# Performance work log

Measured on AMD Instinct MI355X. Metric: run time of the kernel, lower is better.

## Reference

```python
import jax, jax.numpy as jnp
import numpy as np
import math

N_USR = 50000
N_ENT = 100000
D = 64
N_REL = 16
E = 1_000_000
EI = 500_000
N_HEADS = 2


def setup_inputs() -> dict:
    key = jax.random.key(0)
    ks = jax.random.split(key, 9)
    user_emb = jax.random.normal(ks[0], (N_USR, D), jnp.float32) * 0.1
    entity_emb = jax.random.normal(ks[1], (N_ENT, D), jnp.float32) * 0.1
    edge_index = jax.random.randint(ks[2], (2, E), 0, N_ENT, dtype=jnp.int32)
    edge_type = jax.random.randint(ks[3], (E,), 1, N_REL + 1, dtype=jnp.int32)  # values in [1, N_REL]
    inter_u = jax.random.randint(ks[4], (EI,), 0, N_USR, dtype=jnp.int32)
    inter_i = jax.random.randint(ks[5], (EI,), 0, N_ENT, dtype=jnp.int32)
    inter_edge = jnp.stack([inter_u, inter_i], axis=0)
    inter_edge_w = jax.random.uniform(ks[6], (EI,), jnp.float32)
    relation_emb = jax.random.normal(ks[7], (N_REL, D), jnp.float32) * 0.1
    W_Q = jax.random.normal(ks[8], (D, D), jnp.float32) * 0.1
    return {
        'layers_num': 2,
        'user_emb': user_emb,
        'entity_emb': entity_emb,
        'inter_edge': inter_edge,
        'inter_edge_w': inter_edge_w,
        'edge_index': edge_index,
        'edge_type': edge_type,
        'relation_emb': relation_emb,
        'W_Q': W_Q,
    }


def _scatter_softmax(scores, idx, n_segments):
    # scores: [E, H]; softmax over edges sharing the same head index
    m = jax.ops.segment_max(scores, idx, num_segments=n_segments)  # [n, H]
    ex = jnp.exp(scores - m[idx])
    denom = jax.ops.segment_sum(ex, idx, num_segments=n_segments)
    return ex / denom[idx]


def reference(layers_num, user_emb, entity_emb, inter_edge, inter_edge_w, edge_index, edge_type, relation_emb, W_Q):
    n_entities = entity_emb.shape[0]
    n_users = user_emb.shape[0]
    d = entity_emb.shape[1]
    h = N_HEADS
    dk = d // h
    head, tail = edge_index[0], edge_index[1]
    iu, ii = inter_edge[0], inter_edge[1]

    def agg_layer(u_emb, e_emb):
        rel = relation_emb[edge_type - 1]                                # [E, d]
        query = (e_emb[head] @ W_Q).reshape(-1, h, dk)                   # [E, h, dk]
        key = (e_emb[tail] @ W_Q).reshape(-1, h, dk) * rel.reshape(-1, h, dk)
        score = (query * key).sum(-1) / math.sqrt(dk)                    # [E, h]
        attn = _scatter_softmax(score, head, n_entities)                 # [E, h]
        value = (e_emb[tail] * rel).reshape(-1, h, dk)                   # [E, h, dk]
        entity_agg = (value * attn[:, :, None]).reshape(-1, d)           # [E, d]
        entity_agg = jax.ops.segment_sum(entity_agg, head, num_segments=n_entities)
        # F.normalize (L2, eps=1e-12)
        norm = jnp.sqrt(jnp.sum(entity_agg * entity_agg, axis=1, keepdims=True))
        entity_agg = entity_agg / jnp.maximum(norm, 1e-12)
        item_agg = inter_edge_w[:, None] * e_emb[ii]                      # [Ei, d]
        user_agg = jax.ops.segment_sum(item_agg, iu, num_segments=n_users)
        return entity_agg, user_agg

    user_embs = [user_emb]
    entity_embs = [entity_emb]
    u, e = user_emb, entity_emb
    for _ in range(layers_num):
        e, u = agg_layer(u, e)
        user_embs.append(u)
        entity_embs.append(e)
    user_out = jnp.mean(jnp.stack(user_embs, axis=1), axis=1)
    entity_out = jnp.mean(jnp.stack(entity_embs, axis=1), axis=1)
    return (user_out, entity_out)
```

## Files before the change

### kernel.cpp

```cpp
#include <hip/hip_runtime.h>
#include <hip/hip_fp16.h>
#include <math.h>

#define N_USR 50000
#define N_ENT 100000
#define DIM   64
#define NE    1000000
#define NEI   500000

#define BKW   125
#define EBK   800
#define UBK   400
#define CAP   1664
#define KCH   4096
#define NBA_E 245
#define NBA_U 123

#define NBE_B 12500
#define NBU_B 6250

__device__ __forceinline__ __half2 pick_lo(unsigned a, unsigned b) {
    unsigned r = __builtin_amdgcn_perm(b, a, 0x05040100u);
    return *(__half2*)&r;
}
__device__ __forceinline__ __half2 pick_hi(unsigned a, unsigned b) {
    unsigned r = __builtin_amdgcn_perm(b, a, 0x07060302u);
    return *(__half2*)&r;
}

template <int CTRL>
__device__ __forceinline__ float dpp_add(float x) {
    int y = __builtin_amdgcn_update_dpp(0, __builtin_bit_cast(int, x),
                                        CTRL, 0xF, 0xF, true);
    return x + __builtin_bit_cast(float, y);
}

__device__ __forceinline__ int swz16_maxi(int x) {
    int t = __builtin_amdgcn_ds_swizzle(x, 0x401F);
    return max(x, t);
}

typedef _Float16 fp16x2 __attribute__((ext_vector_type(2)));
typedef _Float16 half8 __attribute__((ext_vector_type(8)));
typedef float floatx4 __attribute__((ext_vector_type(4)));

__device__ __forceinline__ float dot2(__half2 a, __half2 b, float c) {
#if __has_builtin(__builtin_amdgcn_fdot2)
    return __builtin_amdgcn_fdot2(__builtin_bit_cast(fp16x2, a),
                                  __builtin_bit_cast(fp16x2, b), c, false);
#else
    __half2 m = __hmul2(a, b);
    return c + __low2float(m) + __high2float(m);
#endif
}

__device__ __forceinline__ float exp2_fast(float x) {
#if __has_builtin(__builtin_amdgcn_exp2f)
    return __builtin_amdgcn_exp2f(x);
#else
    return exp2f(x);
#endif
}

__global__ __launch_bounds__(256) void k_gemm(const float* __restrict__ Emat,
                                              const float* __restrict__ WQ,
                                              unsigned int* __restrict__ Gu,
                                              int ntiles) {
    int lane = threadIdx.x & 63;
    int tile = (int)((blockIdx.x * 256 + threadIdx.x) >> 6);
    if (tile >= ntiles) return;
    int m = lane & 15;
    int g = lane >> 4;
    half8 wf[2][4];
#pragma unroll
    for (int s = 0; s < 2; s++)
#pragma unroll
        for (int t = 0; t < 4; t++)
#pragma unroll
            for (int j = 0; j < 8; j++)
                wf[s][t][j] = (_Float16)WQ[(s * 32 + g * 8 + j) * 64 + t * 16 + m];
    const float* ar = Emat + (size_t)(tile * 16 + m) * 64 + g * 8;
    float4 fa0 = *(const float4*)ar;
    float4 fa1 = *(const float4*)(ar + 4);
    float4 fb0 = *(const float4*)(ar + 32);
    float4 fb1 = *(const float4*)(ar + 36);
    half8 a0, a1;
    a0[0] = (_Float16)fa0.x; a0[1] = (_Float16)fa0.y;
    a0[2] = (_Float16)fa0.z; a0[3] = (_Float16)fa0.w;
    a0[4] = (_Float16)fa1.x; a0[5] = (_Float16)fa1.y;
    a0[6] = (_Float16)fa1.z; a0[7] = (_Float16)fa1.w;
    a1[0] = (_Float16)fb0.x; a1[1] = (_Float16)fb0.y;
    a1[2] = (_Float16)fb0.z; a1[3] = (_Float16)fb0.w;
    a1[4] = (_Float16)fb1.x; a1[5] = (_Float16)fb1.y;
    a1[6] = (_Float16)fb1.z; a1[7] = (_Float16)fb1.w;
    floatx4 acc[4];
#pragma unroll
    for (int t = 0; t < 4; t++) {
        acc[t] = (floatx4){0.f, 0.f, 0.f, 0.f};
        acc[t] = __builtin_amdgcn_mfma_f32_16x16x32_f16(a0, wf[0][t], acc[t], 0, 0, 0);
        acc[t] = __builtin_amdgcn_mfma_f32_16x16x32_f16(a1, wf[1][t], acc[t], 0, 0, 0);
    }
#pragma unroll
    for (int t = 0; t < 4; t++)
#pragma unroll
        for (int r = 0; r < 4; r++) {
            int row = tile * 16 + g * 4 + r;
            int col = t * 16 + m;
            float e = Emat[(size_t)row * 64 + col];
            unsigned short hp = __half_as_ushort(__float2half(acc[t][r]));
            unsigned short he = __half_as_ushort(__float2half(e));
            Gu[(size_t)row * 64 + col] = (unsigned)hp | ((unsigned)he << 16);
        }
}

__global__ __launch_bounds__(256) void k_bucketA(const int* __restrict__ eidx,
                                                 const int* __restrict__ etype,
                                                 const int* __restrict__ inter,
                                                 const float* __restrict__ w,
                                                 int* __restrict__ gcnt,
                                                 int* __restrict__ ebuf,
                                                 int2* __restrict__ ubuf) {
    __shared__ int ch[EBK];
    int tid = threadIdx.x;
    int blk = blockIdx.x;
    for (int j = tid; j < EBK; j += 256) ch[j] = 0;
    __syncthreads();
    if (blk < NBA_E) {
        int lo = blk * KCH, hi = min(lo + KCH, NE);
        for (int i = lo + tid; i < hi; i += 256)
            atomicAdd(&ch[eidx[i] / BKW], 1);
        __syncthreads();
        for (int j = tid; j < EBK; j += 256)
            ch[j] = atomicAdd(&gcnt[j], ch[j]);
        __syncthreads();
        for (int i = lo + tid; i < hi; i += 256) {
            int head = eidx[i];
            int b    = head / BKW;
            int pos  = atomicAdd(&ch[b], 1);
            if (pos < CAP)
                ebuf[b * CAP + pos] = eidx[NE + i] | ((etype[i] - 1) << 20)
                                      | ((head - b * BKW) << 24);
        }
    } else {
        int ub = blk - NBA_E;
        int lo = ub * KCH, hi = min(lo + KCH, NEI);
        for (int i = lo + tid; i < hi; i += 256)
            atomicAdd(&ch[inter[i] / BKW], 1);
        __syncthreads();
        for (int j = tid; j < UBK; j += 256)
            ch[j] = atomicAdd(&gcnt[EBK + j], ch[j]);
        __syncthreads();
        for (int i = lo + tid; i < hi; i += 256) {
            int u   = inter[i];
            int b   = u / BKW;
            int pos = atomicAdd(&ch[b], 1);
            if (pos < CAP)
                ubuf[b * CAP + pos] = make_int2(inter[NEI + i] | ((u - b * BKW) << 24),
                                                __float_as_int(w[i]));
        }
    }
}

__global__ __launch_bounds__(512) void k_bucketB(const int* __restrict__ gcnt,
                                                 const int* __restrict__ ebuf,
                                                 const int2* __restrict__ ubuf,
                                                 int2* __restrict__ off2_e,
                                                 int* __restrict__ edges,
                                                 int2* __restrict__ off2_u,
                                                 int2* __restrict__ iw) {
    __shared__ int h[512];
    __shared__ int cur[512];
    __shared__ int s0[CAP];
    __shared__ int s1[CAP];
    int tid = threadIdx.x;
    int b   = blockIdx.x;
    bool isU = (b >= EBK);
    int lb   = isU ? b - EBK : b;
    int n    = min(gcnt[b], CAP);
    int base = lb * BKW;
    int gbase = lb * CAP;
    h[tid] = 0;
    __syncthreads();
    if (!isU) {
        const int* src = ebuf + (size_t)lb * CAP;
        for (int q = tid; q < n; q += 512) atomicAdd(&h[((unsigned)src[q]) >> 24], 1);
        __syncthreads();
        int v = h[tid];
        for (int d = 1; d < 512; d <<= 1) {
            int x = (tid >= d) ? h[tid - d] : 0;
            __syncthreads();
            h[tid] += x;
            __syncthreads();
        }
        int excl = h[tid] - v;
        cur[tid] = excl;
        if (tid < BKW) off2_e[base + tid] = make_int2(gbase + excl, v);
        __syncthreads();
        for (int q = tid; q < n; q += 512) {
            int x = src[q];
            int r = atomicAdd(&cur[((unsigned)x) >> 24], 1);
            s0[r] = x;
        }
        __syncthreads();
        for (int q = tid; q < n; q += 512) edges[gbase + q] = s0[q] & 0xFFFFFF;
    } else {
        const int2* src = ubuf + (size_t)lb * CAP;
        for (int q = tid; q < n; q += 512) atomicAdd(&h[((unsigned)src[q].x) >> 24], 1);
        __syncthreads();
        int v = h[tid];
        for (int d = 1; d < 512; d <<= 1) {
            int x = (tid >= d) ? h[tid - d] : 0;
            __syncthreads();
            h[tid] += x;
            __syncthreads();
        }
        int excl = h[tid] - v;
        cur[tid] = excl;
        if (tid < BKW) off2_u[base + tid] = make_int2(gbase + excl, v);
        __syncthreads();
        for (int q = tid; q < n; q += 512) {
            int2 x = src[q];
            int r = atomicAdd(&cur[((unsigned)x.x) >> 24], 1);
            s0[r] = x.x;
            s1[r] = x.y;
        }
        __syncthreads();
        for (int q = tid; q < n; q += 512)
            iw[gbase + q] = make_int2(s0[q] & 0xFFFFFF, s1[q]);
    }
}

#define ENT_GATHER(G, R, PK)                                                  \
    {                                                                         \
        G = *(const uint4*)(Gu + (size_t)(unsigned)(PK & 0xFFFFF) * 64 + 4 * dq); \
        R = *(const uint2*)(srel2 + ((((unsigned)PK >> 20) << 5) + dq2));     \
    }

#define ENT_BODY(G, R, KK)                                                    \
    {                                                                         \
        __half2 ra = *(__half2*)&(R).x;                                       \
        __half2 rb = *(__half2*)&(R).y;                                       \
        float sc = dot2(q2a, __hmul2(pick_lo((G).x, (G).y), ra), 0.f);        \
        sc = dot2(q2b, __hmul2(pick_lo((G).z, (G).w), rb), sc);               \
        sc = dpp_add<0xB1>(sc);                                               \
        sc = dpp_add<0x4E>(sc);                                               \
        sc = dpp_add<0x141>(sc);                                              \
        float ex = ((KK) < deg) ? exp2_fast(sc) : 0.f;                        \
        den += ex;                                                            \
        __half2 va = __hmul2(pick_hi((G).x, (G).y), ra);                      \
        __half2 vb = __hmul2(pick_hi((G).z, (G).w), rb);                      \
        acc0 = fmaf(ex, __low2float(va), acc0);                               \
        acc1 = fmaf(ex, __high2float(va), acc1);                              \
        acc2 = fmaf(ex, __low2float(vb), acc2);                               \
        acc3 = fmaf(ex, __high2float(vb), acc3);                              \
    }

__device__ __forceinline__ void ent_path(const unsigned int* __restrict__ Gu,
                                         const unsigned int* srel2,
                                         const int2* __restrict__ off2,
                                         const int* __restrict__ edges,
                                         float* __restrict__ enext,
                                         float* __restrict__ out_ent,
                                         const float* __restrict__ base0,
                                         int mode, int row0, int lane) {
    int grp  = lane >> 4;
    int dq   = lane & 15;
    int dq2  = 2 * dq;
    int row  = row0 + grp;
    uint4 qg = *(const uint4*)(Gu + (size_t)row * 64 + 4 * dq);
    const __half2 qs = __float2half2_rn(0.17677669529663687f * 1.44269504088896340f);
    __half2 q2a = __hmul2(pick_lo(qg.x, qg.y), qs);
    __half2 q2b = __hmul2(pick_lo(qg.z, qg.w), qs);
    int2 od = off2[row];
    int lo = od.x, deg = od.y;
    int km = swz16_maxi(deg);
    km = max(km, __shfl_xor(km, 32, 64));
    float acc0 = 0.f, acc1 = 0.f, acc2 = 0.f, acc3 = 0.f, den = 0.f;
    const int* ep = edges + lo;
    int r0 = ep[0], r1 = ep[1], r2 = ep[2], r3 = ep[3];
    for (int k = 0; k < km; k += 4) {
        int e0v = r0, e1v = r1, e2v = r2, e3v = r3;
        if (k + 4 < km) {
            r0 = ep[k + 4]; r1 = ep[k + 5]; r2 = ep[k + 6]; r3 = ep[k + 7];
        }
        int p0 = (k + 0 < deg) ? e0v : 0;
        int p1 = (k + 1 < deg) ? e1v : 0;
        int p2 = (k + 2 < deg) ? e2v : 0;
        int p3 = (k + 3 < deg) ? e3v : 0;
        bool c1 = (k + 1 < km), c2 = (k + 2 < km), c3 = (k + 3 < km);
        uint4 G0, G1, G2, G3;
        uint2 R0, R1, R2, R3;
        ENT_GATHER(G0, R0, p0);
        if (c1) ENT_GATHER(G1, R1, p1);
        if (c2) ENT_GATHER(G2, R2, p2);
        if (c3) ENT_GATHER(G3, R3, p3);
        ENT_BODY(G0, R0, k);
        if (c1) ENT_BODY(G1, R1, k + 1);
        if (c2) ENT_BODY(G2, R2, k + 2);
        if (c3) ENT_BODY(G3, R3, k + 3);
    }
    float rden = (den > 0.f) ? 1.0f / den : 0.f;
    float rx = acc0 * rden, ry = acc1 * rden, rz = acc2 * rden, rw = acc3 * rden;
    float ss = rx * rx + ry * ry + rz * rz + rw * rw;
    ss = dpp_add<0xB1>(ss);
    ss = dpp_add<0x4E>(ss);
    ss = dpp_add<0x141>(ss);
    ss = dpp_add<0x140>(ss);
    float inv = 1.0f / fmaxf(sqrtf(ss), 1e-12f);
    size_t idx = (size_t)row * 16 + dq;
    float4 y = make_float4(rx * inv, ry * inv, rz * inv, rw * inv);
    if (mode == 0) {
        ((float4*)enext)[idx] = y;
        float4 b0 = ((const float4*)base0)[idx];
        ((float4*)out_ent)[idx] = make_float4(b0.x + y.x, b0.y + y.y,
                                              b0.z + y.z, b0.w + y.w);
    } else {
        float4 o = ((float4*)out_ent)[idx];
        ((float4*)out_ent)[idx] = make_float4((o.x + y.x) * (1.0f / 3.0f),
                                              (o.y + y.y) * (1.0f / 3.0f),
                                              (o.z + y.z) * (1.0f / 3.0f),
                                              (o.w + y.w) * (1.0f / 3.0f));
    }
}

#define USR_BODY(G, WV, KK)                                                   \
    {                                                                         \
        float cw = ((KK) < deg) ? (WV) : 0.f;                                 \
        __half2 h0 = pick_hi((G).x, (G).y);                                   \
        __half2 h1 = pick_hi((G).z, (G).w);                                   \
        acc0 = fmaf(cw, __low2float(h0), acc0);                               \
        acc1 = fmaf(cw, __high2float(h0), acc1);                              \
        acc2 = fmaf(cw, __low2float(h1), acc2);                               \
        acc3 = fmaf(cw, __high2float(h1), acc3);                              \
    }

__device__ __forceinline__ void usr_path(const unsigned int* __restrict__ Gu,
                                         const int2* __restrict__ off2,
                                         const int2* __restrict__ iw,
                                         float* __restrict__ out_user,
                                         const float* __restrict__ base0,
                                         int mode, int row0, int lane) {
    int grp  = lane >> 4;
    int dq   = lane & 15;
    int row  = row0 + grp;
    int2 od = off2[row];
    int lo = od.x, deg = od.y;
    int km = swz16_maxi(deg);
    km = max(km, __shfl_xor(km, 32, 64));
    float acc0 = 0.f, acc1 = 0.f, acc2 = 0.f, acc3 = 0.f;
    const int2* vp = iw + lo;
    int2 v0 = vp[0], v1 = vp[1], v2 = vp[2], v3 = vp[3];
    for (int k = 0; k < km; k += 4) {
        int2 u0 = v0, u1 = v1, u2 = v2, u3 = v3;
        if (k + 4 < km) {
            v0 = vp[k + 4]; v1 = vp[k + 5]; v2 = vp[k + 6]; v3 = vp[k + 7];
        }
        int t0 = (k + 0 < deg) ? u0.x : 0;
        int t1 = (k + 1 < deg) ? u1.x : 0;
        int t2 = (k + 2 < deg) ? u2.x : 0;
        int t3 = (k + 3 < deg) ? u3.x : 0;
        bool c1 = (k + 1 < km), c2 = (k + 2 < km), c3 = (k + 3 < km);
        uint4 g0, g1, g2, g3;
        g0 = *(const uint4*)(Gu + (size_t)t0 * 64 + 4 * dq);
        if (c1) g1 = *(const uint4*)(Gu + (size_t)t1 * 64 + 4 * dq);
        if (c2) g2 = *(const uint4*)(Gu + (size_t)t2 * 64 + 4 * dq);
        if (c3) g3 = *(const uint4*)(Gu + (size_t)t3 * 64 + 4 * dq);
        USR_BODY(g0, __int_as_float(u0.y), k);
        if (c1) USR_BODY(g1, __int_as_float(u1.y), k + 1);
        if (c2) USR_BODY(g2, __int_as_float(u2.y), k + 2);
        if (c3) USR_BODY(g3, __int_as_float(u3.y), k + 3);
    }
    size_t idx = (size_t)row * 16 + dq;
    if (mode == 0) {
        float4 b0 = ((const float4*)base0)[idx];
        ((float4*)out_user)[idx] = make_float4(b0.x + acc0, b0.y + acc1,
                                               b0.z + acc2, b0.w + acc3);
    } else {
        float4 o = ((float4*)out_user)[idx];
        ((float4*)out_user)[idx] = make_float4((o.x + acc0) * (1.0f / 3.0f),
                                               (o.y + acc1) * (1.0f / 3.0f),
                                               (o.z + acc2) * (1.0f / 3.0f),
                                               (o.w + acc3) * (1.0f / 3.0f));
    }
}

__global__ __launch_bounds__(128) void k_agg(const unsigned int* __restrict__ Gu,
                                             const float* __restrict__ rel,
                                             const int2* __restrict__ off2_e,
                                             const int* __restrict__ edges,
                                             const int2* __restrict__ off2_u,
                                             const int2* __restrict__ iw,
                                             float* __restrict__ enext,
                                             float* __restrict__ out_ent,
                                             const float* __restrict__ ent0,
                                             float* __restrict__ out_user,
                                             const float* __restrict__ usr0,
                                             int mode) {
    __shared__ unsigned int srel2[16 * 32];
    int tid = threadIdx.x;
    int b   = blockIdx.x;
    int g   = b / 3;
    int r   = b - 3 * g;
    int lane = tid & 63;
    int wv   = tid >> 6;
    if (r < 2) {
        for (int i = tid; i < 16 * 32; i += 128) {
            float2 rp = ((const float2*)rel)[i];
            __half2 h = __floats2half2_rn(rp.x, rp.y);
            srel2[i] = *(unsigned int*)&h;
        }
        __syncthreads();
        int row0 = (2 * g + r) * 8 + wv * 4;
        ent_path(Gu, srel2, off2_e, edges, enext, out_ent, ent0, mode, row0, lane);
    } else {
        int row0 = g * 8 + wv * 4;
        usr_path(Gu, off2_u, iw, out_user, usr0, mode, row0, lane);
    }
}

extern "C" void kernel_launch(void* const* d_in, const int* in_sizes, int n_in,
                              void* d_out, int out_size, void* d_ws, size_t ws_size,
                              hipStream_t stream) {
    const float* user_emb   = (const float*)d_in[1];
    const float* entity_emb = (const float*)d_in[2];
    const int*   inter_edge = (const int*)d_in[3];
    const float* inter_w    = (const float*)d_in[4];
    const int*   edge_index = (const int*)d_in[5];
    const int*   edge_type  = (const int*)d_in[6];
    const float* rel_emb    = (const float*)d_in[7];
    const float* wq         = (const float*)d_in[8];

    float* out      = (float*)d_out;
    float* out_user = out;
    float* out_ent  = out + (size_t)N_USR * DIM;

    const size_t SZ_E = (size_t)N_ENT * DIM * sizeof(float);
    char* ws = (char*)d_ws;
    size_t o = 0;
#define ALIGN16() o = (o + 15) & ~(size_t)15
    unsigned int* Gu = (unsigned int*)(ws + o); o += (size_t)N_ENT * 64 * 4;
    float* eA      = (float*)(ws + o); o += SZ_E;
    ALIGN16();
    int*   edges   = (int*)  (ws + o); o += ((size_t)EBK * CAP + CAP + 16) * 4;
    ALIGN16();
    int2*  off2_e  = (int2*) (ws + o); o += (size_t)N_ENT * 8;
    ALIGN16();
    int2*  iw      = (int2*) (ws + o); o += ((size_t)UBK * CAP + CAP + 16) * 8;
    int2*  off2_u  = (int2*) (ws + o); o += (size_t)N_USR * 8;
    ALIGN16();
    int*   ebuf    = (int*)  (ws + o); o += (size_t)EBK * CAP * 4;
    ALIGN16();
    int2*  ubuf    = (int2*) (ws + o); o += (size_t)UBK * CAP * 8;
    int*   gcnt    = (int*)  (ws + o); o += (EBK + UBK) * 4;

    hipMemsetAsync(gcnt, 0, (EBK + UBK) * 4, stream);
    k_bucketA<<<NBA_E + NBA_U, 256, 0, stream>>>(edge_index, edge_type,
                                                 inter_edge, inter_w, gcnt,
                                                 ebuf, ubuf);
    k_bucketB<<<EBK + UBK, 512, 0, stream>>>(gcnt, ebuf, ubuf,
                                             off2_e, edges, off2_u, iw);

    const int layers = 2;
    const int ntiles = N_ENT / 16;
    for (int L = 0; L < layers; L++) {
        const float* ecur = (L == 0) ? entity_emb : eA;
        k_gemm<<<(ntiles + 3) / 4, 256, 0, stream>>>(ecur, wq, Gu, ntiles);
        k_agg<<<NBE_B + NBU_B, 128, 0, stream>>>(Gu, rel_emb,
                                                 off2_e, edges, off2_u, iw,
                                                 eA, out_ent, entity_emb,
                                                 out_user, user_emb, L);
    }
}
```

Measured before the change: 296.0 us.

## Add compact fp16 entity copy for user gather and batch bucketing loads

The GEMM kernel now also writes a packed fp16-only copy of the entity embeddings, and the user aggregation path gathers from it. Each lane reads 8 bytes per neighbour instead of the 16-byte interleaved projection/embedding words. The aim is to halve the bytes pulled by the user-path gathers, at the cost of an extra 12.8MB write per layer in the GEMM. Separately, the bucketing kernel preloads its 16 elements per thread into registers once, instead of reading the index arrays twice.

```diff
diff --git a/kernel.cpp b/kernel.cpp
--- a/kernel.cpp
+++ b/kernel.cpp
@@ -65,6 +65,7 @@
 __global__ __launch_bounds__(256) void k_gemm(const float* __restrict__ Emat,
                                               const float* __restrict__ WQ,
                                               unsigned int* __restrict__ Gu,
+                                              __half* __restrict__ Eh,
                                               int ntiles) {
     int lane = threadIdx.x & 63;
     int tile = (int)((blockIdx.x * 256 + threadIdx.x) >> 6);
@@ -110,6 +111,7 @@
             unsigned short hp = __half_as_ushort(__float2half(acc[t][r]));
             unsigned short he = __half_as_ushort(__float2half(e));
             Gu[(size_t)row * 64 + col] = (unsigned)hp | ((unsigned)he << 16);
+            Eh[(size_t)row * 64 + col] = __ushort_as_half(he);
         }
 }
 
@@ -127,37 +129,59 @@
     __syncthreads();
     if (blk < NBA_E) {
         int lo = blk * KCH, hi = min(lo + KCH, NE);
-        for (int i = lo + tid; i < hi; i += 256)
-            atomicAdd(&ch[eidx[i] / BKW], 1);
+        int hd[16], py[16];
+#pragma unroll
+        for (int j = 0; j < 16; j++) {
+            int i = lo + tid + j * 256;
+            bool v = (i < hi);
+            int idx = v ? i : lo;
+            hd[j] = v ? eidx[idx] : -1;
+            py[j] = eidx[NE + idx] | ((etype[idx] - 1) << 20);
+        }
+#pragma unroll
+        for (int j = 0; j < 16; j++)
+            if (hd[j] >= 0) atomicAdd(&ch[hd[j] / BKW], 1);
         __syncthreads();
         for (int j = tid; j < EBK; j += 256)
             ch[j] = atomicAdd(&gcnt[j], ch[j]);
         __syncthreads();
-        for (int i = lo + tid; i < hi; i += 256) {
-            int head = eidx[i];
-            int b    = head / BKW;
-            int pos  = atomicAdd(&ch[b], 1);
-            if (pos < CAP)
-                ebuf[b * CAP + pos] = eidx[NE + i] | ((etype[i] - 1) << 20)
-                                      | ((head - b * BKW) << 24);
-        }
+#pragma unroll
+        for (int j = 0; j < 16; j++)
+            if (hd[j] >= 0) {
+                int b   = hd[j] / BKW;
+                int pos = atomicAdd(&ch[b], 1);
+                if (pos < CAP)
+                    ebuf[b * CAP + pos] = py[j] | ((hd[j] - b * BKW) << 24);
+            }
     } else {
         int ub = blk - NBA_E;
         int lo = ub * KCH, hi = min(lo + KCH, NEI);
-        for (int i = lo + tid; i < hi; i += 256)
-            atomicAdd(&ch[inter[i] / BKW], 1);
+        int ur[16], it[16], wv[16];
+#pragma unroll
+        for (int j = 0; j < 16; j++) {
+            int i = lo + tid + j * 256;
+            bool v = (i < hi);
+            int idx = v ? i : lo;
+            ur[j] = v ? inter[idx] : -1;
+            it[j] = inter[NEI + idx];
+            wv[j] = __float_as_int(w[idx]);
+        }
+#pragma unroll
+        for (int j = 0; j < 16; j++)
+            if (ur[j] >= 0) atomicAdd(&ch[ur[j] / BKW], 1);
         __syncthreads();
         for (int j = tid; j < UBK; j += 256)
             ch[j] = atomicAdd(&gcnt[EBK + j], ch[j]);
         __syncthreads();
-        for (int i = lo + tid; i < hi; i += 256) {
-            int u   = inter[i];
-            int b   = u / BKW;
-            int pos = atomicAdd(&ch[b], 1);
-            if (pos < CAP)
-                ubuf[b * CAP + pos] = make_int2(inter[NEI + i] | ((u - b * BKW) << 24),
-                                                __float_as_int(w[i]));
-        }
+#pragma unroll
+        for (int j = 0; j < 16; j++)
+            if (ur[j] >= 0) {
+                int b   = ur[j] / BKW;
+                int pos = atomicAdd(&ch[b], 1);
+                if (pos < CAP)
+                    ubuf[b * CAP + pos] = make_int2(it[j] | ((ur[j] - b * BKW) << 24),
+                                                    wv[j]);
+            }
     }
 }
 
@@ -326,15 +350,15 @@
 #define USR_BODY(G, WV, KK)                                                   \
     {                                                                         \
         float cw = ((KK) < deg) ? (WV) : 0.f;                                 \
-        __half2 h0 = pick_hi((G).x, (G).y);                                   \
-        __half2 h1 = pick_hi((G).z, (G).w);                                   \
+        __half2 h0 = *(__half2*)&(G).x;                                       \
+        __half2 h1 = *(__half2*)&(G).y;                                       \
         acc0 = fmaf(cw, __low2float(h0), acc0);                               \
         acc1 = fmaf(cw, __high2float(h0), acc1);                              \
         acc2 = fmaf(cw, __low2float(h1), acc2);                               \
         acc3 = fmaf(cw, __high2float(h1), acc3);                              \
     }
 
-__device__ __forceinline__ void usr_path(const unsigned int* __restrict__ Gu,
+__device__ __forceinline__ void usr_path(const unsigned int* __restrict__ Eh2,
                                          const int2* __restrict__ off2,
                                          const int2* __restrict__ iw,
                                          float* __restrict__ out_user,
@@ -342,6 +366,7 @@
                                          int mode, int row0, int lane) {
     int grp  = lane >> 4;
     int dq   = lane & 15;
+    int dq2  = 2 * dq;
     int row  = row0 + grp;
     int2 od = off2[row];
     int lo = od.x, deg = od.y;
@@ -360,11 +385,11 @@
         int t2 = (k + 2 < deg) ? u2.x : 0;
         int t3 = (k + 3 < deg) ? u3.x : 0;
         bool c1 = (k + 1 < km), c2 = (k + 2 < km), c3 = (k + 3 < km);
-        uint4 g0, g1, g2, g3;
-        g0 = *(const uint4*)(Gu + (size_t)t0 * 64 + 4 * dq);
-        if (c1) g1 = *(const uint4*)(Gu + (size_t)t1 * 64 + 4 * dq);
-        if (c2) g2 = *(const uint4*)(Gu + (size_t)t2 * 64 + 4 * dq);
-        if (c3) g3 = *(const uint4*)(Gu + (size_t)t3 * 64 + 4 * dq);
+        uint2 g0, g1, g2, g3;
+        g0 = *(const uint2*)(Eh2 + (size_t)t0 * 32 + dq2);
+        if (c1) g1 = *(const uint2*)(Eh2 + (size_t)t1 * 32 + dq2);
+        if (c2) g2 = *(const uint2*)(Eh2 + (size_t)t2 * 32 + dq2);
+        if (c3) g3 = *(const uint2*)(Eh2 + (size_t)t3 * 32 + dq2);
         USR_BODY(g0, __int_as_float(u0.y), k);
         if (c1) USR_BODY(g1, __int_as_float(u1.y), k + 1);
         if (c2) USR_BODY(g2, __int_as_float(u2.y), k + 2);
@@ -385,6 +410,7 @@
 }
 
 __global__ __launch_bounds__(128) void k_agg(const unsigned int* __restrict__ Gu,
+                                             const unsigned int* __restrict__ Eh2,
                                              const float* __restrict__ rel,
                                              const int2* __restrict__ off2_e,
                                              const int* __restrict__ edges,
@@ -414,7 +440,7 @@
         ent_path(Gu, srel2, off2_e, edges, enext, out_ent, ent0, mode, row0, lane);
     } else {
         int row0 = g * 8 + wv * 4;
-        usr_path(Gu, off2_u, iw, out_user, usr0, mode, row0, lane);
+        usr_path(Eh2, off2_u, iw, out_user, usr0, mode, row0, lane);
     }
 }
 
@@ -439,6 +465,7 @@
     size_t o = 0;
 #define ALIGN16() o = (o + 15) & ~(size_t)15
     unsigned int* Gu = (unsigned int*)(ws + o); o += (size_t)N_ENT * 64 * 4;
+    __half* Eh     = (__half*)(ws + o); o += (size_t)N_ENT * 64 * 2;
     float* eA      = (float*)(ws + o); o += SZ_E;
     ALIGN16();
     int*   edges   = (int*)  (ws + o); o += ((size_t)EBK * CAP + CAP + 16) * 4;
@@ -464,8 +491,8 @@
     const int ntiles = N_ENT / 16;
     for (int L = 0; L < layers; L++) {
         const float* ecur = (L == 0) ? entity_emb : eA;
-        k_gemm<<<(ntiles + 3) / 4, 256, 0, stream>>>(ecur, wq, Gu, ntiles);
-        k_agg<<<NBE_B + NBU_B, 128, 0, stream>>>(Gu, rel_emb,
+        k_gemm<<<(ntiles + 3) / 4, 256, 0, stream>>>(ecur, wq, Gu, Eh, ntiles);
+        k_agg<<<NBE_B + NBU_B, 128, 0, stream>>>(Gu, (const unsigned int*)Eh, rel_emb,
                                                  off2_e, edges, off2_u, iw,
                                                  eA, out_ent, entity_emb,
                                                  out_user, user_emb, L);
```

Result: faster. 275.8 us (-6.8%).
